# Performance work log

Measured on AMD Instinct MI355X. Metric: run time of the kernel, lower is better.

## Reference

```python
import jax, jax.numpy as jnp
import numpy as np

H = 256          # hidden_size
TH_X = 0.05      # delta threshold on inputs
TH_H = 0.05      # delta threshold on hidden state
F_IN = 6         # engineered feature count


def hardswish(v):
    return v * jnp.clip(v + 3.0, 0.0, 6.0) / 6.0


def setup_inputs() -> dict:
    key = jax.random.key(0)
    ks = jax.random.split(key, 6)
    B, T = 32, 4096
    x = jax.random.normal(ks[0], (B, T, 2), dtype=jnp.float32)
    # x2h: Linear(6, 3H, bias=False) -> weight (3H, 6)
    Wx = jax.random.normal(ks[1], (3 * H, F_IN), dtype=jnp.float32) * (1.0 / np.sqrt(F_IN))
    # h2h: Linear(H, 3H, bias=False) -> weight (3H, H)
    Wh = jax.random.normal(ks[2], (3 * H, H), dtype=jnp.float32) * (1.0 / np.sqrt(H))
    # fc_out: Linear(H, 2, bias=False)
    Wo = jax.random.normal(ks[3], (2, H), dtype=jnp.float32) * (1.0 / np.sqrt(H))
    # tcn conv1: Conv1d(2, 3, k=3, padding=16, dilation=16, bias=False) -> (O,I,K)=(3,2,3)
    Wc1 = jax.random.normal(ks[4], (3, 2, 3), dtype=jnp.float32) * 0.3
    # tcn conv2: Conv1d(3, 2, k=1) -> (2,3,1)
    Wc2 = jax.random.normal(ks[5], (2, 3, 1), dtype=jnp.float32) * 0.3
    return {"x": x, "Wx": Wx, "Wh": Wh, "Wo": Wo, "Wc1": Wc1, "Wc2": Wc2}


def _delta_gru(feats_TBF, Wx, Wh):
    # feats_TBF: (T, B, 6). Initial states are always zeros (the torch module
    # resets them whenever x_p_0 is None, which DeltaGRUModel always passes).
    T, B, F = feats_TBF.shape
    dt = feats_TBF.dtype
    carry0 = (
        jnp.zeros((B, F), dt),        # x_p
        jnp.zeros((B, H), dt),        # h
        jnp.zeros((B, H), dt),        # h_p
        jnp.zeros((B, H), dt),        # dm_nh
        jnp.zeros((B, 3 * H), dt),    # dm
    )

    def step(carry, xt):
        x_p, h, h_p, dm_nh, dm = carry
        dx = xt - x_p
        dh = h - h_p
        dxa = jnp.abs(dx)
        dha = jnp.abs(dh)
        dx = jnp.where(dxa < TH_X, 0.0, dx)
        dh = jnp.where(dha < TH_H, 0.0, dh)
        x_p = jnp.where(dxa >= TH_X, xt, x_p)
        h_p = jnp.where(dha >= TH_H, h, h_p)
        mac_x = dx @ Wx.T + dm          # (B, 3H)
        mac_h = dh @ Wh.T               # (B, 3H)
        mxr, mxz, mxn = jnp.split(mac_x, 3, axis=1)
        mhr, mhz, mhn = jnp.split(mac_h, 3, axis=1)
        dm_r = mxr + mhr
        dm_z = mxz + mhz
        dm_n = mxn
        dm_nh = mhn + dm_nh
        dm = jnp.concatenate([dm_r, dm_z, dm_n], axis=1)
        r = jax.nn.sigmoid(dm_r)
        z = jax.nn.sigmoid(dm_z)
        n = jnp.tanh(dm_n + r * dm_nh)
        h = (1.0 - z) * n + z * h
        return (x_p, h, h_p, dm_nh, dm), h

    _, hs = jax.lax.scan(step, carry0, feats_TBF)  # hs: (T, B, H)
    return hs


def reference(x, Wx, Wh, Wo, Wc1, Wc2):
    # x: (B, T, 2)
    B, T, _ = x.shape
    # --- TCN skip path ---
    xc = jnp.transpose(x, (0, 2, 1))  # (B, 2, T)
    c1 = jax.lax.conv_general_dilated(
        xc, Wc1, window_strides=(1,), padding=[(16, 16)], rhs_dilation=(16,),
        dimension_numbers=("NCH", "OIH", "NCH"))
    c2 = jax.lax.conv_general_dilated(
        hardswish(c1), Wc2, window_strides=(1,), padding=[(0, 0)],
        dimension_numbers=("NCH", "OIH", "NCH"))
    skip = jnp.transpose(hardswish(c2), (0, 2, 1))  # (B, T, 2)
    # --- engineered features ---
    i = x[..., 0:1]
    q = x[..., 1:2]
    amp2 = i * i + q * q
    amp = jnp.sqrt(jnp.maximum(amp2, 1e-12))
    amp3 = amp * amp2
    i_prev = jnp.pad(i[:, :-1, :], ((0, 0), (1, 0), (0, 0)))
    q_prev = jnp.pad(q[:, :-1, :], ((0, 0), (1, 0), (0, 0)))
    feats = jnp.concatenate([i, q, amp, amp3, i_prev, q_prev], axis=-1)  # (B,T,6)
    # --- delta-GRU scan (time-major) ---
    hs = _delta_gru(jnp.transpose(feats, (1, 0, 2)), Wx, Wh)  # (T, B, H)
    out = jnp.transpose(hs, (1, 0, 2))  # (B, T, H)
    return out @ Wo.T + skip  # (B, T, 2)
```

## Files before the change

kernel.cpp:

```cpp
#include <hip/hip_runtime.h>
#include <math.h>

#define HH 256
#define FIN 6
#define TT 4096
#define BB 32
#define TH 0.05f

typedef _Float16 h2 __attribute__((ext_vector_type(2)));
typedef int iv64 __attribute__((ext_vector_type(64)));
struct H8 { h2 a, b, c, d; };

__device__ __forceinline__ int packh2(float a, float b) {
    h2 v = { (_Float16)a, (_Float16)b };
    return __builtin_bit_cast(int, v);
}
__device__ __forceinline__ h2 toh2(int x) { return __builtin_bit_cast(h2, x); }

__device__ __forceinline__ float hswish(float v) {
    float c = fminf(fmaxf(v + 3.0f, 0.0f), 6.0f);
    return v * c * (1.0f / 6.0f);
}
__device__ __forceinline__ float fexp2(float x) { return __builtin_amdgcn_exp2f(x); }
__device__ __forceinline__ float frcp(float x)  { return __builtin_amdgcn_rcpf(x); }
__device__ __forceinline__ float sigm(float x)  { return frcp(1.0f + fexp2(-1.44269504f * x)); }
__device__ __forceinline__ float tanhf_fast(float x) {
    float ax = fabsf(x);
    float e = fexp2(2.88539008f * ax);
    float t = 1.0f - 2.0f * frcp(e + 1.0f);
    return copysignf(t, x);
}

__global__ __launch_bounds__(256) void k_prep(
        const float* __restrict__ x, const float* __restrict__ Wc1,
        const float* __restrict__ Wc2, float* __restrict__ feats,
        float* __restrict__ out) {
    int idx = blockIdx.x * 256 + threadIdx.x;
    if (idx >= BB * TT) return;
    int b = idx >> 12;
    int t = idx & (TT - 1);
    const float* xb = x + (size_t)b * TT * 2;
    float i0 = xb[t * 2 + 0], q0 = xb[t * 2 + 1];
    float ip = (t > 0) ? xb[(t - 1) * 2 + 0] : 0.0f;
    float qp = (t > 0) ? xb[(t - 1) * 2 + 1] : 0.0f;
    float amp2 = i0 * i0 + q0 * q0;
    float amp  = sqrtf(fmaxf(amp2, 1e-12f));
    float amp3 = amp * amp2;
    float* f = feats + (size_t)idx * 6;
    f[0] = i0; f[1] = q0; f[2] = amp; f[3] = amp3; f[4] = ip; f[5] = qp;

    float c1[3];
#pragma unroll
    for (int m = 0; m < 3; m++) {
        float acc = 0.0f;
#pragma unroll
        for (int k = 0; k < 3; k++) {
            int tt = t + (k - 1) * 16;
            if (tt >= 0 && tt < TT) {
                acc += Wc1[m * 6 + 0 * 3 + k] * xb[tt * 2 + 0];
                acc += Wc1[m * 6 + 1 * 3 + k] * xb[tt * 2 + 1];
            }
        }
        c1[m] = hswish(acc);
    }
#pragma unroll
    for (int o = 0; o < 2; o++) {
        float acc = Wc2[o * 3 + 0] * c1[0] + Wc2[o * 3 + 1] * c1[1] + Wc2[o * 3 + 2] * c1[2];
        out[(size_t)idx * 2 + o] = hswish(acc);
    }
}

__global__ __attribute__((amdgpu_flat_work_group_size(512, 512), amdgpu_waves_per_eu(2, 2)))
void k_gru(
        const float* __restrict__ feats, const float* __restrict__ Wx,
        const float* __restrict__ Wh, const float* __restrict__ Wo,
        float* __restrict__ out) {
    __shared__ float s_out[TT * 2];
    __shared__ __align__(16) _Float16 s_dhh[2][HH];
    __shared__ __align__(16) float s_dx[2][8];
    __shared__ float s_feat[2][128 * FIN];

    const int tid  = threadIdx.x;
    const int wv   = tid >> 6;
    const int lane = tid & 63;
    const int half = lane >> 5;
    const int row  = wv * 32 + (lane & 31);
    const int b    = blockIdx.x;
    const float* fb = feats + (size_t)b * TT * FIN;

    for (int i = tid; i < TT * 2; i += 512) s_out[i] = 0.0f;
    for (int i = tid; i < 128 * FIN; i += 512) s_feat[0][i] = fb[i];

    iv64 wrv{}, wzv{}, wnv{};
    {
        const int k0 = half * 128;
        const float4* p0 = (const float4*)(Wh + (size_t)(0 * HH + row) * HH + k0);
        const float4* p1 = (const float4*)(Wh + (size_t)(1 * HH + row) * HH + k0);
        const float4* p2 = (const float4*)(Wh + (size_t)(2 * HH + row) * HH + k0);
#pragma unroll
        for (int c = 0; c < 32; c++) {
            float4 v0 = p0[c], v1 = p1[c], v2 = p2[c];
            wrv[2 * c]     = packh2(v0.x, v0.y);
            wrv[2 * c + 1] = packh2(v0.z, v0.w);
            wzv[2 * c]     = packh2(v1.x, v1.y);
            wzv[2 * c + 1] = packh2(v1.z, v1.w);
            wnv[2 * c]     = packh2(v2.x, v2.y);
            wnv[2 * c + 1] = packh2(v2.z, v2.w);
        }
    }
    float wxr[FIN], wxz[FIN], wxn[FIN];
#pragma unroll
    for (int f = 0; f < FIN; f++) {
        wxr[f] = Wx[(size_t)(0 * HH + row) * FIN + f];
        wxz[f] = Wx[(size_t)(1 * HH + row) * FIN + f];
        wxn[f] = Wx[(size_t)(2 * HH + row) * FIN + f];
    }
    const float woc = Wo[half * HH + row];

    float h = 0.0f, hp = 0.0f, dmr = 0.0f, dmz = 0.0f, dmn = 0.0f, dmnh = 0.0f;
    float xp = 0.0f, curf = 0.0f;
    if (tid < FIN) curf = fb[tid];

    __syncthreads();

#pragma unroll 1
    for (int t = 0; t < TT; t++) {
        const int tb = t & 1;

        if ((t & 127) == 64 && t + 64 < TT) {
            const int w = (t >> 7) + 1;
#pragma unroll 1
            for (int i = tid; i < 128 * FIN; i += 512)
                s_feat[w & 1][i] = fb[(size_t)w * 128 * FIN + i];
        }

        {
            float dh = h - hp;
            bool keep = fabsf(dh) >= TH;
            if (half == 0) s_dhh[tb][row] = (_Float16)(keep ? dh : 0.0f);
            if (keep) hp = h;
        }
        if (tid < FIN) {
            float dx = curf - xp;
            bool keep = fabsf(dx) >= TH;
            s_dx[tb][tid] = keep ? dx : 0.0f;
            if (keep) xp = curf;
        }
        __syncthreads();

        float mxr = dmr, mxz = dmz, mxn = dmn;
        {
            const float4* dx4 = (const float4*)s_dx[tb];
            float4 da = dx4[0], db = dx4[1];
            mxr = fmaf(da.x, wxr[0], mxr); mxz = fmaf(da.x, wxz[0], mxz); mxn = fmaf(da.x, wxn[0], mxn);
            mxr = fmaf(da.y, wxr[1], mxr); mxz = fmaf(da.y, wxz[1], mxz); mxn = fmaf(da.y, wxn[1], mxn);
            mxr = fmaf(da.z, wxr[2], mxr); mxz = fmaf(da.z, wxz[2], mxz); mxn = fmaf(da.z, wxn[2], mxn);
            mxr = fmaf(da.w, wxr[3], mxr); mxz = fmaf(da.w, wxz[3], mxz); mxn = fmaf(da.w, wxn[3], mxn);
            mxr = fmaf(db.x, wxr[4], mxr); mxz = fmaf(db.x, wxz[4], mxz); mxn = fmaf(db.x, wxn[4], mxn);
            mxr = fmaf(db.y, wxr[5], mxr); mxz = fmaf(db.y, wxz[5], mxz); mxn = fmaf(db.y, wxn[5], mxn);
        }
        float ar = 0.0f, az = 0.0f, an = 0.0f;
        {
            const H8* dp = (const H8*)s_dhh[tb] + half * 16;
#pragma unroll
            for (int c = 0; c < 16; c++) {
                H8 d = dp[c];
                ar = __builtin_amdgcn_fdot2(d.a, toh2(wrv[4 * c + 0]), ar, false);
                az = __builtin_amdgcn_fdot2(d.a, toh2(wzv[4 * c + 0]), az, false);
                an = __builtin_amdgcn_fdot2(d.a, toh2(wnv[4 * c + 0]), an, false);
                ar = __builtin_amdgcn_fdot2(d.b, toh2(wrv[4 * c + 1]), ar, false);
                az = __builtin_amdgcn_fdot2(d.b, toh2(wzv[4 * c + 1]), az, false);
                an = __builtin_amdgcn_fdot2(d.b, toh2(wnv[4 * c + 1]), an, false);
                ar = __builtin_amdgcn_fdot2(d.c, toh2(wrv[4 * c + 2]), ar, false);
                az = __builtin_amdgcn_fdot2(d.c, toh2(wzv[4 * c + 2]), az, false);
                an = __builtin_amdgcn_fdot2(d.c, toh2(wnv[4 * c + 2]), an, false);
                ar = __builtin_amdgcn_fdot2(d.d, toh2(wrv[4 * c + 3]), ar, false);
                az = __builtin_amdgcn_fdot2(d.d, toh2(wzv[4 * c + 3]), az, false);
                an = __builtin_amdgcn_fdot2(d.d, toh2(wnv[4 * c + 3]), an, false);
            }
        }
        ar += __shfl_xor(ar, 32, 64);
        az += __shfl_xor(az, 32, 64);
        an += __shfl_xor(an, 32, 64);

        dmr = mxr + ar;
        dmz = mxz + az;
        dmn = mxn;
        dmnh += an;

        {
            float r = sigm(dmr);
            float z = sigm(dmz);
            float nn = tanhf_fast(dmn + r * dmnh);
            h = (1.0f - z) * nn + z * h;
        }

        {
            float p = h * woc;
            p += __shfl_xor(p, 16, 64);
            p += __shfl_xor(p, 8, 64);
            p += __shfl_xor(p, 4, 64);
            p += __shfl_xor(p, 2, 64);
            p += __shfl_xor(p, 1, 64);
            if ((lane & 31) == 0) atomicAdd(&s_out[2 * t + half], p);
        }

        if (tid < FIN && t + 1 < TT) {
            const int tn = t + 1;
            curf = s_feat[(tn >> 7) & 1][(tn & 127) * FIN + tid];
        }
    }

    __syncthreads();
    const size_t outbase = (size_t)b * TT * 2;
    for (int i = tid; i < TT * 2; i += 512) out[outbase + i] += s_out[i];
}

extern "C" void kernel_launch(void* const* d_in, const int* in_sizes, int n_in,
                              void* d_out, int out_size, void* d_ws, size_t ws_size,
                              hipStream_t stream) {
    const float* x   = (const float*)d_in[0];
    const float* Wx  = (const float*)d_in[1];
    const float* Wh  = (const float*)d_in[2];
    const float* Wo  = (const float*)d_in[3];
    const float* Wc1 = (const float*)d_in[4];
    const float* Wc2 = (const float*)d_in[5];
    float* out = (float*)d_out;
    float* feats = (float*)d_ws;

    k_prep<<<(BB * TT + 255) / 256, 256, 0, stream>>>(x, Wc1, Wc2, feats, out);
    k_gru<<<BB, 512, 0, stream>>>(feats, Wx, Wh, Wo, out);
}
```

Before: 5.220 ms.

## Split GRU hidden matvec across four lane groups with 1024-thread blocks

```diff
diff --git a/kernel.cpp b/kernel.cpp
--- a/kernel.cpp
+++ b/kernel.cpp
@@ -8,7 +8,7 @@
 #define TH 0.05f
 
 typedef _Float16 h2 __attribute__((ext_vector_type(2)));
-typedef int iv64 __attribute__((ext_vector_type(64)));
+typedef int iv32 __attribute__((ext_vector_type(32)));
 struct H8 { h2 a, b, c, d; };
 
 __device__ __forceinline__ int packh2(float a, float b) {
@@ -70,35 +70,38 @@
     }
 }
 
-__global__ __attribute__((amdgpu_flat_work_group_size(512, 512), amdgpu_waves_per_eu(2, 2)))
+__global__ __attribute__((amdgpu_flat_work_group_size(1024, 1024), amdgpu_waves_per_eu(4, 4)))
 void k_gru(
         const float* __restrict__ feats, const float* __restrict__ Wx,
         const float* __restrict__ Wh, const float* __restrict__ Wo,
         float* __restrict__ out) {
     __shared__ float s_out[TT * 2];
     __shared__ __align__(16) _Float16 s_dhh[2][HH];
-    __shared__ __align__(16) float s_dx[2][8];
+    __shared__ __align__(16) float s_dxf[2][8];
+    __shared__ float s_xp[8];
     __shared__ float s_feat[2][128 * FIN];
 
     const int tid  = threadIdx.x;
     const int wv   = tid >> 6;
     const int lane = tid & 63;
-    const int half = lane >> 5;
-    const int row  = wv * 32 + (lane & 31);
+    const int q    = lane >> 4;
+    const int sub  = lane & 15;
+    const int row  = wv * 16 + sub;
     const int b    = blockIdx.x;
     const float* fb = feats + (size_t)b * TT * FIN;
 
-    for (int i = tid; i < TT * 2; i += 512) s_out[i] = 0.0f;
-    for (int i = tid; i < 128 * FIN; i += 512) s_feat[0][i] = fb[i];
-
-    iv64 wrv{}, wzv{}, wnv{};
+    for (int i = tid; i < TT * 2; i += 1024) s_out[i] = 0.0f;
+    if (tid < 128 * FIN) s_feat[0][tid] = fb[tid];
+    if (tid < 8) { s_xp[tid] = 0.0f; s_dxf[0][tid] = 0.0f; s_dxf[1][tid] = 0.0f; }
+
+    iv32 wrv{}, wzv{}, wnv{};
     {
-        const int k0 = half * 128;
+        const int k0 = q * 64;
         const float4* p0 = (const float4*)(Wh + (size_t)(0 * HH + row) * HH + k0);
         const float4* p1 = (const float4*)(Wh + (size_t)(1 * HH + row) * HH + k0);
         const float4* p2 = (const float4*)(Wh + (size_t)(2 * HH + row) * HH + k0);
 #pragma unroll
-        for (int c = 0; c < 32; c++) {
+        for (int c = 0; c < 16; c++) {
             float4 v0 = p0[c], v1 = p1[c], v2 = p2[c];
             wrv[2 * c]     = packh2(v0.x, v0.y);
             wrv[2 * c + 1] = packh2(v0.z, v0.w);
@@ -108,18 +111,16 @@
             wnv[2 * c + 1] = packh2(v2.z, v2.w);
         }
     }
-    float wxr[FIN], wxz[FIN], wxn[FIN];
-#pragma unroll
-    for (int f = 0; f < FIN; f++) {
-        wxr[f] = Wx[(size_t)(0 * HH + row) * FIN + f];
-        wxz[f] = Wx[(size_t)(1 * HH + row) * FIN + f];
-        wxn[f] = Wx[(size_t)(2 * HH + row) * FIN + f];
-    }
-    const float woc = Wo[half * HH + row];
+    const int f0 = 2 * q, f1 = 2 * q + 1;
+    const float wxr0 = (f0 < FIN) ? Wx[(size_t)(0 * HH + row) * FIN + f0] : 0.0f;
+    const float wxr1 = (f1 < FIN) ? Wx[(size_t)(0 * HH + row) * FIN + f1] : 0.0f;
+    const float wxz0 = (f0 < FIN) ? Wx[(size_t)(1 * HH + row) * FIN + f0] : 0.0f;
+    const float wxz1 = (f1 < FIN) ? Wx[(size_t)(1 * HH + row) * FIN + f1] : 0.0f;
+    const float wxn0 = (f0 < FIN) ? Wx[(size_t)(2 * HH + row) * FIN + f0] : 0.0f;
+    const float wxn1 = (f1 < FIN) ? Wx[(size_t)(2 * HH + row) * FIN + f1] : 0.0f;
+    const float woc  = (q == 0) ? Wo[row] : ((q == 1) ? Wo[HH + row] : 0.0f);
 
     float h = 0.0f, hp = 0.0f, dmr = 0.0f, dmz = 0.0f, dmn = 0.0f, dmnh = 0.0f;
-    float xp = 0.0f, curf = 0.0f;
-    if (tid < FIN) curf = fb[tid];
 
     __syncthreads();
 
@@ -129,64 +130,61 @@
 
         if ((t & 127) == 64 && t + 64 < TT) {
             const int w = (t >> 7) + 1;
-#pragma unroll 1
-            for (int i = tid; i < 128 * FIN; i += 512)
-                s_feat[w & 1][i] = fb[(size_t)w * 128 * FIN + i];
+            if (tid < 128 * FIN)
+                s_feat[w & 1][tid] = fb[(size_t)w * 128 * FIN + tid];
         }
 
         {
             float dh = h - hp;
             bool keep = fabsf(dh) >= TH;
-            if (half == 0) s_dhh[tb][row] = (_Float16)(keep ? dh : 0.0f);
+            if (q == 0) s_dhh[tb][row] = (_Float16)(keep ? dh : 0.0f);
             if (keep) hp = h;
         }
         if (tid < FIN) {
-            float dx = curf - xp;
-            bool keep = fabsf(dx) >= TH;
-            s_dx[tb][tid] = keep ? dx : 0.0f;
-            if (keep) xp = curf;
+            float fcur = s_feat[(t >> 7) & 1][(t & 127) * FIN + tid];
+            float xp = s_xp[tid];
+            float dxv = fcur - xp;
+            bool keep = fabsf(dxv) >= TH;
+            s_dxf[tb][tid] = keep ? dxv : 0.0f;
+            if (keep) s_xp[tid] = fcur;
         }
         __syncthreads();
 
-        float mxr = dmr, mxz = dmz, mxn = dmn;
-        {
-            const float4* dx4 = (const float4*)s_dx[tb];
-            float4 da = dx4[0], db = dx4[1];
-            mxr = fmaf(da.x, wxr[0], mxr); mxz = fmaf(da.x, wxz[0], mxz); mxn = fmaf(da.x, wxn[0], mxn);
-            mxr = fmaf(da.y, wxr[1], mxr); mxz = fmaf(da.y, wxz[1], mxz); mxn = fmaf(da.y, wxn[1], mxn);
-            mxr = fmaf(da.z, wxr[2], mxr); mxz = fmaf(da.z, wxz[2], mxz); mxn = fmaf(da.z, wxn[2], mxn);
-            mxr = fmaf(da.w, wxr[3], mxr); mxz = fmaf(da.w, wxz[3], mxz); mxn = fmaf(da.w, wxn[3], mxn);
-            mxr = fmaf(db.x, wxr[4], mxr); mxz = fmaf(db.x, wxz[4], mxz); mxn = fmaf(db.x, wxn[4], mxn);
-            mxr = fmaf(db.y, wxr[5], mxr); mxz = fmaf(db.y, wxz[5], mxz); mxn = fmaf(db.y, wxn[5], mxn);
-        }
-        float ar = 0.0f, az = 0.0f, an = 0.0f;
-        {
-            const H8* dp = (const H8*)s_dhh[tb] + half * 16;
-#pragma unroll
-            for (int c = 0; c < 16; c++) {
+        float ar, az, anx, anh = 0.0f;
+        {
+            float dxa = s_dxf[tb][f0], dxb = s_dxf[tb][f1];
+            ar  = dxa * wxr0; ar  = fmaf(dxb, wxr1, ar);
+            az  = dxa * wxz0; az  = fmaf(dxb, wxz1, az);
+            anx = dxa * wxn0; anx = fmaf(dxb, wxn1, anx);
+        }
+        {
+            const H8* dp = (const H8*)(s_dhh[tb] + (q << 6));
+#pragma unroll
+            for (int c = 0; c < 8; c++) {
                 H8 d = dp[c];
-                ar = __builtin_amdgcn_fdot2(d.a, toh2(wrv[4 * c + 0]), ar, false);
-                az = __builtin_amdgcn_fdot2(d.a, toh2(wzv[4 * c + 0]), az, false);
-                an = __builtin_amdgcn_fdot2(d.a, toh2(wnv[4 * c + 0]), an, false);
-                ar = __builtin_amdgcn_fdot2(d.b, toh2(wrv[4 * c + 1]), ar, false);
-                az = __builtin_amdgcn_fdot2(d.b, toh2(wzv[4 * c + 1]), az, false);
-                an = __builtin_amdgcn_fdot2(d.b, toh2(wnv[4 * c + 1]), an, false);
-                ar = __builtin_amdgcn_fdot2(d.c, toh2(wrv[4 * c + 2]), ar, false);
-                az = __builtin_amdgcn_fdot2(d.c, toh2(wzv[4 * c + 2]), az, false);
-                an = __builtin_amdgcn_fdot2(d.c, toh2(wnv[4 * c + 2]), an, false);
-                ar = __builtin_amdgcn_fdot2(d.d, toh2(wrv[4 * c + 3]), ar, false);
-                az = __builtin_amdgcn_fdot2(d.d, toh2(wzv[4 * c + 3]), az, false);
-                an = __builtin_amdgcn_fdot2(d.d, toh2(wnv[4 * c + 3]), an, false);
+                ar  = __builtin_amdgcn_fdot2(d.a, toh2(wrv[4 * c + 0]), ar,  false);
+                az  = __builtin_amdgcn_fdot2(d.a, toh2(wzv[4 * c + 0]), az,  false);
+                anh = __builtin_amdgcn_fdot2(d.a, toh2(wnv[4 * c + 0]), anh, false);
+                ar  = __builtin_amdgcn_fdot2(d.b, toh2(wrv[4 * c + 1]), ar,  false);
+                az  = __builtin_amdgcn_fdot2(d.b, toh2(wzv[4 * c + 1]), az,  false);
+                anh = __builtin_amdgcn_fdot2(d.b, toh2(wnv[4 * c + 1]), anh, false);
+                ar  = __builtin_amdgcn_fdot2(d.c, toh2(wrv[4 * c + 2]), ar,  false);
+                az  = __builtin_amdgcn_fdot2(d.c, toh2(wzv[4 * c + 2]), az,  false);
+                anh = __builtin_amdgcn_fdot2(d.c, toh2(wnv[4 * c + 2]), anh, false);
+                ar  = __builtin_amdgcn_fdot2(d.d, toh2(wrv[4 * c + 3]), ar,  false);
+                az  = __builtin_amdgcn_fdot2(d.d, toh2(wzv[4 * c + 3]), az,  false);
+                anh = __builtin_amdgcn_fdot2(d.d, toh2(wnv[4 * c + 3]), anh, false);
             }
         }
-        ar += __shfl_xor(ar, 32, 64);
-        az += __shfl_xor(az, 32, 64);
-        an += __shfl_xor(an, 32, 64);
-
-        dmr = mxr + ar;
-        dmz = mxz + az;
-        dmn = mxn;
-        dmnh += an;
+        ar  += __shfl_xor(ar, 16, 64);  ar  += __shfl_xor(ar, 32, 64);
+        az  += __shfl_xor(az, 16, 64);  az  += __shfl_xor(az, 32, 64);
+        anx += __shfl_xor(anx, 16, 64); anx += __shfl_xor(anx, 32, 64);
+        anh += __shfl_xor(anh, 16, 64); anh += __shfl_xor(anh, 32, 64);
+
+        dmr  += ar;
+        dmz  += az;
+        dmn  += anx;
+        dmnh += anh;
 
         {
             float r = sigm(dmr);
@@ -197,23 +195,17 @@
 
         {
             float p = h * woc;
-            p += __shfl_xor(p, 16, 64);
+            p += __shfl_xor(p, 1, 64);
+            p += __shfl_xor(p, 2, 64);
+            p += __shfl_xor(p, 4, 64);
             p += __shfl_xor(p, 8, 64);
-            p += __shfl_xor(p, 4, 64);
-            p += __shfl_xor(p, 2, 64);
-            p += __shfl_xor(p, 1, 64);
-            if ((lane & 31) == 0) atomicAdd(&s_out[2 * t + half], p);
-        }
-
-        if (tid < FIN && t + 1 < TT) {
-            const int tn = t + 1;
-            curf = s_feat[(tn >> 7) & 1][(tn & 127) * FIN + tid];
+            if (sub == 0 && q < 2) atomicAdd(&s_out[2 * t + q], p);
         }
     }
 
     __syncthreads();
     const size_t outbase = (size_t)b * TT * 2;
-    for (int i = tid; i < TT * 2; i += 512) out[outbase + i] += s_out[i];
+    for (int i = tid; i < TT * 2; i += 1024) out[outbase + i] += s_out[i];
 }
 
 extern "C" void kernel_launch(void* const* d_in, const int* in_sizes, int n_in,
@@ -229,5 +221,5 @@
     float* feats = (float*)d_ws;
 
     k_prep<<<(BB * TT + 255) / 256, 256, 0, stream>>>(x, Wc1, Wc2, feats, out);
-    k_gru<<<BB, 512, 0, stream>>>(feats, Wx, Wh, Wo, out);
-}
+    k_gru<<<BB, 1024, 0, stream>>>(feats, Wx, Wh, Wo, out);
+}
```

New measurement: 6.859 ms. 31.4% more time.

## Split each batch row's GRU across two workgroups with flag-synchronized delta exchange

Applied to the files above, without the earlier changes.

```diff
diff --git a/kernel.cpp b/kernel.cpp
--- a/kernel.cpp
+++ b/kernel.cpp
@@ -7,6 +7,9 @@
 #define BB 32
 #define TH 0.05f
 
+#define EXO (3 * 1024 * 1024)
+#define FLO (EXO + 32 * 1024)
+
 typedef _Float16 h2 __attribute__((ext_vector_type(2)));
 typedef int iv64 __attribute__((ext_vector_type(64)));
 struct H8 { h2 a, b, c, d; };
@@ -16,7 +19,9 @@
     return __builtin_bit_cast(int, v);
 }
 __device__ __forceinline__ h2 toh2(int x) { return __builtin_bit_cast(h2, x); }
-
+__device__ __forceinline__ float fdot2(h2 a, h2 b, float c) {
+    return __builtin_amdgcn_fdot2(a, b, c, false);
+}
 __device__ __forceinline__ float hswish(float v) {
     float c = fminf(fmaxf(v + 3.0f, 0.0f), 6.0f);
     return v * c * (1.0f / 6.0f);
@@ -34,8 +39,9 @@
 __global__ __launch_bounds__(256) void k_prep(
         const float* __restrict__ x, const float* __restrict__ Wc1,
         const float* __restrict__ Wc2, float* __restrict__ feats,
-        float* __restrict__ out) {
+        float* __restrict__ out, char* __restrict__ ws) {
     int idx = blockIdx.x * 256 + threadIdx.x;
+    if (idx < 2048) ((int*)(ws + FLO))[idx] = 0;
     if (idx >= BB * TT) return;
     int b = idx >> 12;
     int t = idx & (TT - 1);
@@ -70,52 +76,63 @@
     }
 }
 
-__global__ __attribute__((amdgpu_flat_work_group_size(512, 512), amdgpu_waves_per_eu(2, 2)))
-void k_gru(
+__device__ __forceinline__ iv64 load_pack64(const float* rowptr) {
+    iv64 v{};
+    const float4* p = (const float4*)rowptr;
+#pragma unroll
+    for (int c = 0; c < 32; c++) {
+        float4 t = p[c];
+        v[2 * c]     = packh2(t.x, t.y);
+        v[2 * c + 1] = packh2(t.z, t.w);
+    }
+    return v;
+}
+
+__global__ __launch_bounds__(256, 1) void k_gru(
         const float* __restrict__ feats, const float* __restrict__ Wx,
         const float* __restrict__ Wh, const float* __restrict__ Wo,
-        float* __restrict__ out) {
+        float* __restrict__ out, char* __restrict__ ws) {
     __shared__ float s_out[TT * 2];
     __shared__ __align__(16) _Float16 s_dhh[2][HH];
     __shared__ __align__(16) float s_dx[2][8];
     __shared__ float s_feat[2][128 * FIN];
 
     const int tid  = threadIdx.x;
+    const int bb   = blockIdx.x;
+    const int b    = bb & 31;
+    const int sub  = bb >> 5;
     const int wv   = tid >> 6;
     const int lane = tid & 63;
     const int half = lane >> 5;
-    const int row  = wv * 32 + (lane & 31);
-    const int b    = blockIdx.x;
+    const int jl   = lane & 31;
+    const int j    = wv * 32 + jl;
+    const int hrow = sub * 128 + j;
+    const int k0   = half * 128;
+
     const float* fb = feats + (size_t)b * TT * FIN;
-
-    for (int i = tid; i < TT * 2; i += 512) s_out[i] = 0.0f;
-    for (int i = tid; i < 128 * FIN; i += 512) s_feat[0][i] = fb[i];
-
-    iv64 wrv{}, wzv{}, wnv{};
-    {
-        const int k0 = half * 128;
-        const float4* p0 = (const float4*)(Wh + (size_t)(0 * HH + row) * HH + k0);
-        const float4* p1 = (const float4*)(Wh + (size_t)(1 * HH + row) * HH + k0);
-        const float4* p2 = (const float4*)(Wh + (size_t)(2 * HH + row) * HH + k0);
-#pragma unroll
-        for (int c = 0; c < 32; c++) {
-            float4 v0 = p0[c], v1 = p1[c], v2 = p2[c];
-            wrv[2 * c]     = packh2(v0.x, v0.y);
-            wrv[2 * c + 1] = packh2(v0.z, v0.w);
-            wzv[2 * c]     = packh2(v1.x, v1.y);
-            wzv[2 * c + 1] = packh2(v1.z, v1.w);
-            wnv[2 * c]     = packh2(v2.x, v2.y);
-            wnv[2 * c + 1] = packh2(v2.z, v2.w);
-        }
-    }
-    float wxr[FIN], wxz[FIN], wxn[FIN];
-#pragma unroll
-    for (int f = 0; f < FIN; f++) {
-        wxr[f] = Wx[(size_t)(0 * HH + row) * FIN + f];
-        wxz[f] = Wx[(size_t)(1 * HH + row) * FIN + f];
-        wxn[f] = Wx[(size_t)(2 * HH + row) * FIN + f];
-    }
-    const float woc = Wo[half * HH + row];
+    ushort* ex = (ushort*)(ws + EXO);
+    int* flags = (int*)(ws + FLO);
+    ushort* ex_out = ex + (size_t)((b * 2 + sub) * 2) * 128;
+    const ushort* ex_in = ex + (size_t)((b * 2 + (1 - sub)) * 2) * 128;
+    int* myflag = flags + (b * 2 + sub) * 32;
+    int* pflag  = flags + (b * 2 + (1 - sub)) * 32;
+
+    for (int i = tid; i < TT * 2; i += 256) s_out[i] = 0.0f;
+    for (int i = tid; i < 128 * FIN; i += 256) s_feat[0][i] = fb[i];
+
+    const iv64 wrv = load_pack64(Wh + (size_t)(0 * HH + hrow) * HH + k0);
+    const iv64 wzv = load_pack64(Wh + (size_t)(1 * HH + hrow) * HH + k0);
+    const iv64 wnv = load_pack64(Wh + (size_t)(2 * HH + hrow) * HH + k0);
+
+    const int f0 = half * 3;
+    float wxr[3], wxz[3], wxn[3];
+#pragma unroll
+    for (int i = 0; i < 3; i++) {
+        wxr[i] = Wx[(size_t)(0 * HH + hrow) * FIN + f0 + i];
+        wxz[i] = Wx[(size_t)(1 * HH + hrow) * FIN + f0 + i];
+        wxn[i] = Wx[(size_t)(2 * HH + hrow) * FIN + f0 + i];
+    }
+    const float woc = Wo[half * HH + hrow];
 
     float h = 0.0f, hp = 0.0f, dmr = 0.0f, dmz = 0.0f, dmn = 0.0f, dmnh = 0.0f;
     float xp = 0.0f, curf = 0.0f;
@@ -129,16 +146,20 @@
 
         if ((t & 127) == 64 && t + 64 < TT) {
             const int w = (t >> 7) + 1;
-#pragma unroll 1
-            for (int i = tid; i < 128 * FIN; i += 512)
+            for (int i = tid; i < 128 * FIN; i += 256)
                 s_feat[w & 1][i] = fb[(size_t)w * 128 * FIN + i];
         }
 
         {
             float dh = h - hp;
             bool keep = fabsf(dh) >= TH;
-            if (half == 0) s_dhh[tb][row] = (_Float16)(keep ? dh : 0.0f);
+            float dhv = keep ? dh : 0.0f;
             if (keep) hp = h;
+            if (half == 0) {
+                _Float16 dq = (_Float16)dhv;
+                s_dhh[tb][hrow] = dq;
+                ex_out[tb * 128 + j] = __builtin_bit_cast(ushort, dq);
+            }
         }
         if (tid < FIN) {
             float dx = curf - xp;
@@ -148,45 +169,51 @@
         }
         __syncthreads();
 
-        float mxr = dmr, mxz = dmz, mxn = dmn;
-        {
-            const float4* dx4 = (const float4*)s_dx[tb];
-            float4 da = dx4[0], db = dx4[1];
-            mxr = fmaf(da.x, wxr[0], mxr); mxz = fmaf(da.x, wxz[0], mxz); mxn = fmaf(da.x, wxn[0], mxn);
-            mxr = fmaf(da.y, wxr[1], mxr); mxz = fmaf(da.y, wxz[1], mxz); mxn = fmaf(da.y, wxn[1], mxn);
-            mxr = fmaf(da.z, wxr[2], mxr); mxz = fmaf(da.z, wxz[2], mxz); mxn = fmaf(da.z, wxn[2], mxn);
-            mxr = fmaf(da.w, wxr[3], mxr); mxz = fmaf(da.w, wxz[3], mxz); mxn = fmaf(da.w, wxn[3], mxn);
-            mxr = fmaf(db.x, wxr[4], mxr); mxz = fmaf(db.x, wxz[4], mxz); mxn = fmaf(db.x, wxn[4], mxn);
-            mxr = fmaf(db.y, wxr[5], mxr); mxz = fmaf(db.y, wxz[5], mxz); mxn = fmaf(db.y, wxn[5], mxn);
-        }
-        float ar = 0.0f, az = 0.0f, an = 0.0f;
+        if (tid == 192)
+            __hip_atomic_store(myflag, t + 1, __ATOMIC_RELEASE, __HIP_MEMORY_SCOPE_AGENT);
+        if (tid < 16) {
+            while (__hip_atomic_load(pflag, __ATOMIC_ACQUIRE, __HIP_MEMORY_SCOPE_AGENT) < t + 1) {}
+            uint4 v = ((const uint4*)(ex_in + tb * 128))[tid];
+            ((uint4*)&s_dhh[tb][(1 - sub) * 128])[tid] = v;
+        }
+        __syncthreads();
+
+        float ar, az, anx, anh = 0.0f;
+        {
+            const float* dxp = s_dx[tb];
+            float d0 = dxp[f0 + 0], d1 = dxp[f0 + 1], d2 = dxp[f0 + 2];
+            ar  = d0 * wxr[0]; ar  = fmaf(d1, wxr[1], ar);  ar  = fmaf(d2, wxr[2], ar);
+            az  = d0 * wxz[0]; az  = fmaf(d1, wxz[1], az);  az  = fmaf(d2, wxz[2], az);
+            anx = d0 * wxn[0]; anx = fmaf(d1, wxn[1], anx); anx = fmaf(d2, wxn[2], anx);
+        }
         {
             const H8* dp = (const H8*)s_dhh[tb] + half * 16;
 #pragma unroll
             for (int c = 0; c < 16; c++) {
                 H8 d = dp[c];
-                ar = __builtin_amdgcn_fdot2(d.a, toh2(wrv[4 * c + 0]), ar, false);
-                az = __builtin_amdgcn_fdot2(d.a, toh2(wzv[4 * c + 0]), az, false);
-                an = __builtin_amdgcn_fdot2(d.a, toh2(wnv[4 * c + 0]), an, false);
-                ar = __builtin_amdgcn_fdot2(d.b, toh2(wrv[4 * c + 1]), ar, false);
-                az = __builtin_amdgcn_fdot2(d.b, toh2(wzv[4 * c + 1]), az, false);
-                an = __builtin_amdgcn_fdot2(d.b, toh2(wnv[4 * c + 1]), an, false);
-                ar = __builtin_amdgcn_fdot2(d.c, toh2(wrv[4 * c + 2]), ar, false);
-                az = __builtin_amdgcn_fdot2(d.c, toh2(wzv[4 * c + 2]), az, false);
-                an = __builtin_amdgcn_fdot2(d.c, toh2(wnv[4 * c + 2]), an, false);
-                ar = __builtin_amdgcn_fdot2(d.d, toh2(wrv[4 * c + 3]), ar, false);
-                az = __builtin_amdgcn_fdot2(d.d, toh2(wzv[4 * c + 3]), az, false);
-                an = __builtin_amdgcn_fdot2(d.d, toh2(wnv[4 * c + 3]), an, false);
+                ar  = fdot2(d.a, toh2(wrv[4 * c + 0]), ar);
+                az  = fdot2(d.a, toh2(wzv[4 * c + 0]), az);
+                anh = fdot2(d.a, toh2(wnv[4 * c + 0]), anh);
+                ar  = fdot2(d.b, toh2(wrv[4 * c + 1]), ar);
+                az  = fdot2(d.b, toh2(wzv[4 * c + 1]), az);
+                anh = fdot2(d.b, toh2(wnv[4 * c + 1]), anh);
+                ar  = fdot2(d.c, toh2(wrv[4 * c + 2]), ar);
+                az  = fdot2(d.c, toh2(wzv[4 * c + 2]), az);
+                anh = fdot2(d.c, toh2(wnv[4 * c + 2]), anh);
+                ar  = fdot2(d.d, toh2(wrv[4 * c + 3]), ar);
+                az  = fdot2(d.d, toh2(wzv[4 * c + 3]), az);
+                anh = fdot2(d.d, toh2(wnv[4 * c + 3]), anh);
             }
         }
-        ar += __shfl_xor(ar, 32, 64);
-        az += __shfl_xor(az, 32, 64);
-        an += __shfl_xor(an, 32, 64);
-
-        dmr = mxr + ar;
-        dmz = mxz + az;
-        dmn = mxn;
-        dmnh += an;
+        ar  += __shfl_xor(ar, 32, 64);
+        az  += __shfl_xor(az, 32, 64);
+        anx += __shfl_xor(anx, 32, 64);
+        anh += __shfl_xor(anh, 32, 64);
+
+        dmr  += ar;
+        dmz  += az;
+        dmn  += anx;
+        dmnh += anh;
 
         {
             float r = sigm(dmr);
@@ -197,12 +224,12 @@
 
         {
             float p = h * woc;
+            p += __shfl_xor(p, 1, 64);
+            p += __shfl_xor(p, 2, 64);
+            p += __shfl_xor(p, 4, 64);
+            p += __shfl_xor(p, 8, 64);
             p += __shfl_xor(p, 16, 64);
-            p += __shfl_xor(p, 8, 64);
-            p += __shfl_xor(p, 4, 64);
-            p += __shfl_xor(p, 2, 64);
-            p += __shfl_xor(p, 1, 64);
-            if ((lane & 31) == 0) atomicAdd(&s_out[2 * t + half], p);
+            if (jl == 0) atomicAdd(&s_out[2 * t + half], p);
         }
 
         if (tid < FIN && t + 1 < TT) {
@@ -213,7 +240,8 @@
 
     __syncthreads();
     const size_t outbase = (size_t)b * TT * 2;
-    for (int i = tid; i < TT * 2; i += 512) out[outbase + i] += s_out[i];
+    for (int i = tid; i < TT * 2; i += 256)
+        atomicAdd(&out[outbase + i], s_out[i]);
 }
 
 extern "C" void kernel_launch(void* const* d_in, const int* in_sizes, int n_in,
@@ -227,7 +255,8 @@
     const float* Wc2 = (const float*)d_in[5];
     float* out = (float*)d_out;
     float* feats = (float*)d_ws;
-
-    k_prep<<<(BB * TT + 255) / 256, 256, 0, stream>>>(x, Wc1, Wc2, feats, out);
-    k_gru<<<BB, 512, 0, stream>>>(feats, Wx, Wh, Wo, out);
-}
+    char* ws = (char*)d_ws;
+
+    k_prep<<<(BB * TT + 255) / 256, 256, 0, stream>>>(x, Wc1, Wc2, feats, out, ws);
+    k_gru<<<64, 256, 0, stream>>>(feats, Wx, Wh, Wo, out, ws);
+}
```

Measured after the change: 10.62 ms. 103% more time.
